# Optimization experiments

Measured on AMD Instinct MI355X. Metric: run time of the kernel, lower is better.

Reference implementation:

```python
import jax, jax.numpy as jnp
import numpy as np

B, T, D = 2, 2048, 1024
N_HEADS, N_KV_HEADS = 16, 4
D_HEAD = D // N_HEADS            # 64
N_GROUPS = N_HEADS // N_KV_HEADS  # 4
ROPE_THETA = 10000.0


def _rope_freqs(t, d_head, theta):
    inv = 1.0 / (theta ** (jnp.arange(0, d_head, 2, dtype=jnp.float32) / d_head))  # (d_head/2,)
    ang = jnp.arange(t, dtype=jnp.float32)[:, None] * inv[None, :]                 # (T, d_head/2)
    return jnp.stack([jnp.cos(ang), jnp.sin(ang)], axis=-1)                        # (T, d_head/2, 2)


def _apply_rope(x, freqs):
    # x: (B, T, H, d_head); freqs: (T, d_head/2, 2) = (cos, sin)
    xr = x.reshape(*x.shape[:-1], -1, 2)          # (B,T,H,d/2,2)
    xre, xim = xr[..., 0], xr[..., 1]
    fre = freqs[None, :, None, :, 0]              # (1,T,1,d/2)
    fim = freqs[None, :, None, :, 1]
    outre = xre * fre - xim * fim
    outim = xre * fim + xim * fre
    return jnp.stack([outre, outim], axis=-1).reshape(x.shape)


def setup_inputs() -> dict:
    key = jax.random.key(0)
    ks = jax.random.split(key, 5)
    x = jax.random.normal(ks[0], (B, T, D), dtype=jnp.float32)
    w_q = jax.random.normal(ks[1], (N_HEADS * D_HEAD, D), dtype=jnp.float32) * 0.02
    w_k = jax.random.normal(ks[2], (N_KV_HEADS * D_HEAD, D), dtype=jnp.float32) * 0.02
    w_v = jax.random.normal(ks[3], (N_KV_HEADS * D_HEAD, D), dtype=jnp.float32) * 0.02
    w_o = jax.random.normal(ks[4], (D, N_HEADS * D_HEAD), dtype=jnp.float32) * 0.02
    rope_freqs = _rope_freqs(T, D_HEAD, ROPE_THETA)
    causal = jnp.tril(jnp.ones((T, T), dtype=bool))
    mask = jnp.where(causal, 0.0, -1e9).astype(jnp.float32)[None, None]  # (1,1,T,T)
    return {"x": x, "rope_freqs": rope_freqs, "mask": mask,
            "w_q": w_q, "w_k": w_k, "w_v": w_v, "w_o": w_o}


def reference(x, rope_freqs, mask, w_q, w_k, w_v, w_o):
    # projections (torch Linear: y = x @ W.T)
    q = jnp.einsum('btd,od->bto', x, w_q).reshape(B, T, N_HEADS, D_HEAD)
    k = jnp.einsum('btd,od->bto', x, w_k).reshape(B, T, N_KV_HEADS, D_HEAD)
    v = jnp.einsum('btd,od->bto', x, w_v).reshape(B, T, N_KV_HEADS, D_HEAD)
    q = _apply_rope(q, rope_freqs)
    k = _apply_rope(k, rope_freqs)
    # GQA: expand KV heads (kv head h -> N_GROUPS contiguous query heads)
    k = jnp.repeat(k, N_GROUPS, axis=2)   # (B,T,H,d)
    v = jnp.repeat(v, N_GROUPS, axis=2)
    q = q.transpose(0, 2, 1, 3)           # (B,H,T,d)
    k = k.transpose(0, 2, 1, 3)
    v = v.transpose(0, 2, 1, 3)
    scale = 1.0 / np.sqrt(D_HEAD).astype(np.float32)
    scores = jnp.einsum('bhqd,bhkd->bhqk', q, k) * scale + mask
    attn = jax.nn.softmax(scores, axis=-1)
    out = jnp.einsum('bhqk,bhkd->bhqd', attn, v)
    out = out.transpose(0, 2, 1, 3).reshape(B, T, N_HEADS * D_HEAD)
    return jnp.einsum('bto,do->btd', out, w_o)
```

## Files before the change

### kernel.cpp

```cpp
#include <hip/hip_runtime.h>
#include <hip/hip_bf16.h>
#include <cstddef>
#include <type_traits>

#define TT   2048
#define NH   16
#define NKV  4
#define DH   64

typedef __bf16 bf16x8 __attribute__((ext_vector_type(8)));
typedef float  f32x4  __attribute__((ext_vector_type(4)));

#if __has_builtin(__builtin_amdgcn_exp2f)
#define EXP2F(x) __builtin_amdgcn_exp2f(x)
#else
#define EXP2F(x) __expf((x) * 0.69314718056f)
#endif

#define QSCALE 0.180336880f

__device__ __forceinline__ void gl_lds16(const __bf16* g, __bf16* l)
{
    __builtin_amdgcn_global_load_lds(
        (const __attribute__((address_space(1))) void*)g,
        (__attribute__((address_space(3))) void*)l,
        16, 0, 0);
}

__global__ __launch_bounds__(256)
void cast_kernel(const float* __restrict__ x,  const float* __restrict__ wq,
                 const float* __restrict__ wk, const float* __restrict__ wv,
                 const float* __restrict__ wo,
                 __bf16* __restrict__ xb, __bf16* __restrict__ wqkv,
                 __bf16* __restrict__ wob)
{
    const int g = blockIdx.x * 256 + threadIdx.x;
    const float* src;
    __bf16* dst;
    int off;
    if (g < 1048576)       { src = x;  dst = xb;   off = g; }
    else if (g < 1310720)  { src = wq; dst = wqkv; off = g - 1048576; }
    else if (g < 1376256)  { src = wk; dst = wqkv + 1048576; off = g - 1310720; }
    else if (g < 1441792)  { src = wv; dst = wqkv + 1310720; off = g - 1376256; }
    else                   { src = wo; dst = wob;  off = g - 1441792; }
    const float4 v = *(const float4*)(src + (size_t)off * 4);
    union { __bf16 h[4]; uint2 u; } o;
    o.h[0] = (__bf16)v.x; o.h[1] = (__bf16)v.y;
    o.h[2] = (__bf16)v.z; o.h[3] = (__bf16)v.w;
    *(uint2*)(dst + (size_t)off * 4) = o.u;
}

template<int MODE>
__global__ __launch_bounds__(256, 3)
void mm_kernel(const __bf16* __restrict__ A,
               const __bf16* __restrict__ W,
               const float* __restrict__ rope,
               void* __restrict__ O0, void* __restrict__ O1,
               void* __restrict__ O2)
{
    constexpr int K  = 1024;
    constexpr int NK = K / 32;
    constexpr int NX = (MODE == 0) ? 12 : 8;
    __shared__ __bf16 As[2][64 * 32];
    __shared__ __bf16 Bs[2][128 * 32];

    const int tid  = threadIdx.x;
    const int lane = tid & 63;
    const int wv   = tid >> 6;
    const int quad = lane >> 4;
    const int lc   = lane & 15;
    const int wbase = tid & 192;

    const int dlin = blockIdx.x + NX * blockIdx.y;
    const int nid  = (dlin & 7) * ((NX * 64) >> 3) + (dlin >> 3);
    const int bx   = nid % NX;
    const int by   = nid / NX;

    const int gm0  = by * 64;
    const int gn0  = bx * 128;
    const int wc0  = wv * 32;

    size_t gaA;
    {
        const int p = tid;
        const int r = p >> 2, q = (p & 3) ^ ((r >> 1) & 3);
        gaA = (size_t)r * K + q * 8;
    }
    size_t gaB[2];
#pragma unroll
    for (int j = 0; j < 2; j++) {
        const int p = tid + j * 256;
        const int r = p >> 2, q = (p & 3) ^ ((r >> 1) & 3);
        gaB[j] = (size_t)r * K + q * 8;
    }
    const __bf16* Ag = A + (size_t)gm0 * K;
    const __bf16* Wg = W + (size_t)gn0 * K;

    auto foff = [&](int row) { return (row * 4 + (quad ^ ((row >> 1) & 3))) * 8; };
    int aoff[4], boff[2];
#pragma unroll
    for (int i = 0; i < 4; i++) aoff[i] = foff(i * 16 + lc);
#pragma unroll
    for (int j = 0; j < 2; j++) boff[j] = foff(wc0 + j * 16 + lc);

    f32x4 acc[4][2];
#pragma unroll
    for (int i = 0; i < 4; i++)
#pragma unroll
        for (int j = 0; j < 2; j++) acc[i][j] = (f32x4){0.f, 0.f, 0.f, 0.f};

    auto stage = [&](int s, int kt) {
        const int kb = kt * 32;
        gl_lds16(Ag + gaA + kb, &As[s][wbase * 8]);
        gl_lds16(Wg + gaB[0] + kb, &Bs[s][wbase * 8]);
        gl_lds16(Wg + gaB[1] + kb, &Bs[s][(wbase + 256) * 8]);
    };

    stage(0, 0);
    __syncthreads();

    for (int kt = 0; kt < NK; kt++) {
        const int P = kt & 1;
        if (kt + 1 < NK) stage(P ^ 1, kt + 1);

        bf16x8 af[4], bfr[2];
#pragma unroll
        for (int i = 0; i < 4; i++) af[i]  = *(const bf16x8*)&As[P][aoff[i]];
#pragma unroll
        for (int j = 0; j < 2; j++) bfr[j] = *(const bf16x8*)&Bs[P][boff[j]];
#pragma unroll
        for (int i = 0; i < 4; i++)
#pragma unroll
            for (int j = 0; j < 2; j++)
                acc[i][j] = __builtin_amdgcn_mfma_f32_16x16x32_bf16(
                    af[i], bfr[j], acc[i][j], 0, 0, 0);

        if (kt + 1 < NK) __syncthreads();
    }

    if (MODE == 0) {
        __bf16* Qo = (__bf16*)O0;
        __bf16* Ko = (__bf16*)O1;
        __bf16* Vo = (__bf16*)O2;
        const int region = (gn0 < 1024) ? 0 : (gn0 < 1280) ? 1 : 2;
#pragma unroll
        for (int i = 0; i < 4; i++) {
#pragma unroll
            for (int r = 0; r < 4; r++) {
                const int grow = gm0 + i * 16 + quad * 4 + r;
                const int b = grow >> 11, t = grow & 2047;
                const float* rrow = rope + t * 64;
#pragma unroll
                for (int j = 0; j < 2; j++) {
                    const float v = acc[i][j][r];
                    const float partner = __shfl_xor(v, 1, 64);
                    const int col = gn0 + wc0 + j * 16 + lc;
                    if (region == 0) {
                        const int h = col >> 6, d = col & 63;
                        const float2 cs = *(const float2*)(rrow + (d >> 1) * 2);
                        const float out = v * cs.x + partner * ((d & 1) ? cs.y : -cs.y);
                        Qo[((size_t)(b * NH + h) * TT + t) * DH + d] = (__bf16)(out * QSCALE);
                    } else if (region == 1) {
                        const int ck = col - 1024;
                        const int kh = ck >> 6, d = ck & 63;
                        const float2 cs = *(const float2*)(rrow + (d >> 1) * 2);
                        const float out = v * cs.x + partner * ((d & 1) ? cs.y : -cs.y);
                        Ko[((size_t)(b * NKV + kh) * TT + t) * DH + d] = (__bf16)out;
                    } else {
                        const int cv = col - 1280;
                        const int kh = cv >> 6, d = cv & 63;
                        Vo[((size_t)(b * NKV + kh) * DH + d) * TT + t] = (__bf16)v;
                    }
                }
            }
        }
    } else {
        float* Of = (float*)O0;
#pragma unroll
        for (int i = 0; i < 4; i++)
#pragma unroll
            for (int r = 0; r < 4; r++) {
                const int grow = gm0 + i * 16 + quad * 4 + r;
#pragma unroll
                for (int j = 0; j < 2; j++)
                    Of[(size_t)grow * 1024 + gn0 + wc0 + j * 16 + lc] = acc[i][j][r];
            }
    }
}

__global__ __launch_bounds__(256, 4)
void attn_kernel(const __bf16* __restrict__ Q,
                 const __bf16* __restrict__ K,
                 const __bf16* __restrict__ Vt,
                 __bf16* __restrict__ O)
{
    __shared__ __bf16 Ks[2][64 * 64];
    __shared__ __bf16 Vs[2][64 * 64];
    __shared__ __bf16 Ps[4][16][64];

    const int tid  = threadIdx.x;
    const int lane = tid & 63;
    const int wv   = tid >> 6;
    const int quad = lane >> 4;
    const int lc   = lane & 15;

    const int a   = blockIdx.x & 31;
    const int rep = blockIdx.x >> 5;
    const int qt  = ((rep >> 3) & 1) ? (31 - a) : a;
    const int b   = rep >> 4;
    const int h   = rep & 15;
    const int kh  = h >> 2;
    const int nk  = qt + 1;

    const __bf16* Kg = K  + (size_t)(b * NKV + kh) * TT * DH;
    const __bf16* Vg = Vt + (size_t)(b * NKV + kh) * DH * TT;

    bf16x8 qb[2];
    {
        const __bf16* qp = Q + ((size_t)(b * NH + h) * TT
                                + qt * 64 + wv * 16 + lc) * DH;
        qb[0] = *(const bf16x8*)(qp + quad * 8);
        qb[1] = *(const bf16x8*)(qp + 32 + quad * 8);
    }

    int koff[2], voff[2], lsl[2];
#pragma unroll
    for (int j = 0; j < 2; j++) {
        const int p  = tid + j * 256;
        const int r  = p >> 3;
        const int qs = (p & 7) ^ (r & 7);
        koff[j] = r * DH + qs * 8;
        voff[j] = r * TT + qs * 8;
        lsl[j]  = p * 8;
    }

    int foff[4][2];
#pragma unroll
    for (int g = 0; g < 4; g++)
#pragma unroll
        for (int c = 0; c < 2; c++)
            foff[g][c] = ((g * 16 + lc) * 8 + ((c * 4 + quad) ^ (lc & 7))) * 8;

    const int psw = 2 * (lc & 7);
    char* prow = (char*)&Ps[wv][lc][0];

    float l_s = 0.f;
    f32x4 oacc[4];
#pragma unroll
    for (int g = 0; g < 4; g++) oacc[g] = (f32x4){0.f, 0.f, 0.f, 0.f};

    bf16x8 kr[2], vr[2];
    auto load_regs = [&](int kt) {
        const __bf16* kp = Kg + (size_t)kt * 64 * DH;
        const __bf16* vp = Vg + (size_t)kt * 64;
#pragma unroll
        for (int j = 0; j < 2; j++) {
            kr[j] = *(const bf16x8*)(kp + koff[j]);
            vr[j] = *(const bf16x8*)(vp + voff[j]);
        }
    };
    auto store_lds = [&](int buf) {
#pragma unroll
        for (int j = 0; j < 2; j++) {
            *(bf16x8*)&Ks[buf][lsl[j]] = kr[j];
            *(bf16x8*)&Vs[buf][lsl[j]] = vr[j];
        }
    };

    load_regs(0);
    store_lds(0);
    if (nk > 1) load_regs(1);
    __syncthreads();

    for (int kt = 0; kt < nk; kt++) {
        const int cur = kt & 1;

        bf16x8 ka[4][2];
#pragma unroll
        for (int g = 0; g < 4; g++) {
            ka[g][0] = *(const bf16x8*)&Ks[cur][foff[g][0]];
            ka[g][1] = *(const bf16x8*)&Ks[cur][foff[g][1]];
        }

        if (kt + 1 < nk) store_lds(cur ^ 1);

        const int D = qt * 64 + wv * 16 - kt * 64;

        f32x4 s[4];
        __builtin_amdgcn_s_setprio(1);
#pragma unroll
        for (int g = 0; g < 4; g++) {
            f32x4 z = (f32x4){0.f, 0.f, 0.f, 0.f};
            z = __builtin_amdgcn_mfma_f32_16x16x32_bf16(ka[g][0], qb[0], z, 0, 0, 0);
            z = __builtin_amdgcn_mfma_f32_16x16x32_bf16(ka[g][1], qb[1], z, 0, 0, 0);
            s[g] = z;
        }
        __builtin_amdgcn_s_setprio(0);

        if (D < 63) {
            const int thr = D + lc;
#pragma unroll
            for (int g = 0; g < 4; g++)
#pragma unroll
                for (int r = 0; r < 4; r++)
                    if (g * 16 + quad * 4 + r > thr) s[g][r] = -1e30f;
        }

        float rs = 0.f;
#pragma unroll
        for (int g = 0; g < 4; g++) {
#pragma unroll
            for (int r = 0; r < 4; r++) {
                s[g][r] = EXP2F(s[g][r]);
                rs += s[g][r];
            }
            union { __bf16 hh[4]; uint2 uu; } pk;
            pk.hh[0] = (__bf16)s[g][0]; pk.hh[1] = (__bf16)s[g][1];
            pk.hh[2] = (__bf16)s[g][2]; pk.hh[3] = (__bf16)s[g][3];
            *(uint2*)(prow + ((4 * g + quad) ^ psw) * 8) = pk.uu;
        }
        l_s += rs;

        bf16x8 va[4][2];
#pragma unroll
        for (int g = 0; g < 4; g++) {
            va[g][0] = *(const bf16x8*)&Vs[cur][foff[g][0]];
            va[g][1] = *(const bf16x8*)&Vs[cur][foff[g][1]];
        }

        const bf16x8 pb0 = *(const bf16x8*)(prow + (( 2 * quad) ^ psw) * 8);
        const bf16x8 pb1 = *(const bf16x8*)(prow + ((8 + 2 * quad) ^ psw) * 8);
        __builtin_amdgcn_s_setprio(1);
#pragma unroll
        for (int g = 0; g < 4; g++) {
            oacc[g] = __builtin_amdgcn_mfma_f32_16x16x32_bf16(va[g][0], pb0, oacc[g], 0, 0, 0);
            oacc[g] = __builtin_amdgcn_mfma_f32_16x16x32_bf16(va[g][1], pb1, oacc[g], 0, 0, 0);
        }
        __builtin_amdgcn_s_setprio(0);

        if (kt + 2 < nk) load_regs(kt + 2);
        if (kt + 1 < nk) __syncthreads();
    }

    {
        float l = l_s;
        l += __shfl_xor(l, 16, 64);
        l += __shfl_xor(l, 32, 64);
        const float inv = 1.f / l;
        const int t = qt * 64 + wv * 16 + lc;
        __bf16* op = O + (size_t)(b * TT + t) * (NH * DH) + h * DH;
#pragma unroll
        for (int g = 0; g < 4; g++) {
            union { __bf16 hh[4]; uint2 uu; } pk;
            pk.hh[0] = (__bf16)(oacc[g][0] * inv);
            pk.hh[1] = (__bf16)(oacc[g][1] * inv);
            pk.hh[2] = (__bf16)(oacc[g][2] * inv);
            pk.hh[3] = (__bf16)(oacc[g][3] * inv);
            *(uint2*)(op + g * 16 + quad * 4) = pk.uu;
        }
    }
}

extern "C" void kernel_launch(void* const* d_in, const int* in_sizes, int n_in,
                              void* d_out, int out_size, void* d_ws, size_t ws_size,
                              hipStream_t stream)
{
    const float* x    = (const float*)d_in[0];
    const float* rope = (const float*)d_in[1];
    const float* w_q  = (const float*)d_in[3];
    const float* w_k  = (const float*)d_in[4];
    const float* w_v  = (const float*)d_in[5];
    const float* w_o  = (const float*)d_in[6];
    float* out = (float*)d_out;

    char* ws = (char*)d_ws;
    __bf16* Qb   = (__bf16*)(ws);
    __bf16* Kb   = (__bf16*)(ws + (8  << 20));
    __bf16* Vtb  = (__bf16*)(ws + (10 << 20));
    __bf16* AOb  = (__bf16*)(ws + (12 << 20));
    __bf16* xb   = (__bf16*)(ws + (20 << 20));
    __bf16* Wqkv = (__bf16*)(ws + (28 << 20));
    __bf16* Wob  = (__bf16*)(ws + (31 << 20));

    cast_kernel<<<6656, dim3(256), 0, stream>>>(x, w_q, w_k, w_v, w_o,
                                                xb, Wqkv, Wob);

    dim3 g1(12, 64);
    mm_kernel<0><<<g1, dim3(256), 0, stream>>>(xb, Wqkv, rope,
                                               (void*)Qb, (void*)Kb, (void*)Vtb);

    attn_kernel<<<1024, dim3(256), 0, stream>>>(Qb, Kb, Vtb, AOb);

    dim3 g3(8, 64);
    mm_kernel<1><<<g3, dim3(256), 0, stream>>>(AOb, Wob, rope,
                                               (void*)out, nullptr, nullptr);
}
```

Baseline: 174.8 us.

## Shrink GEMM tiles to 64x64 and replace LDS-direct loads with register-staged pipeline

The projection GEMMs switch from 64x128 tiles to 64x64 tiles, which doubles the number of workgroups and raises the occupancy hint to 4 per CU. The direct global-to-LDS loads are replaced by global loads into registers, prefetched three k-steps ahead and written to a double-buffered LDS, with the loop unrolled by two. The intent is more parallelism across CUs and better hiding of load latency. In exchange, each tile gets less data reuse (more global traffic per MFMA) and the kernel uses more VGPRs.

```diff
diff --git a/kernel.cpp b/kernel.cpp
--- a/kernel.cpp
+++ b/kernel.cpp
@@ -18,14 +18,6 @@
 #endif
 
 #define QSCALE 0.180336880f
-
-__device__ __forceinline__ void gl_lds16(const __bf16* g, __bf16* l)
-{
-    __builtin_amdgcn_global_load_lds(
-        (const __attribute__((address_space(1))) void*)g,
-        (__attribute__((address_space(3))) void*)l,
-        16, 0, 0);
-}
 
 __global__ __launch_bounds__(256)
 void cast_kernel(const float* __restrict__ x,  const float* __restrict__ wq,
@@ -51,7 +43,7 @@
 }
 
 template<int MODE>
-__global__ __launch_bounds__(256, 3)
+__global__ __launch_bounds__(256, 4)
 void mm_kernel(const __bf16* __restrict__ A,
                const __bf16* __restrict__ W,
                const float* __restrict__ rope,
@@ -60,82 +52,83 @@
 {
     constexpr int K  = 1024;
     constexpr int NK = K / 32;
-    constexpr int NX = (MODE == 0) ? 12 : 8;
+    constexpr int NX = (MODE == 0) ? 24 : 16;
+    constexpr int NWG = NX * 64;
     __shared__ __bf16 As[2][64 * 32];
-    __shared__ __bf16 Bs[2][128 * 32];
+    __shared__ __bf16 Bs[2][64 * 32];
 
     const int tid  = threadIdx.x;
     const int lane = tid & 63;
     const int wv   = tid >> 6;
     const int quad = lane >> 4;
     const int lc   = lane & 15;
-    const int wbase = tid & 192;
 
     const int dlin = blockIdx.x + NX * blockIdx.y;
-    const int nid  = (dlin & 7) * ((NX * 64) >> 3) + (dlin >> 3);
+    const int nid  = (dlin & 7) * (NWG >> 3) + (dlin >> 3);
     const int bx   = nid % NX;
     const int by   = nid / NX;
 
     const int gm0  = by * 64;
-    const int gn0  = bx * 128;
-    const int wc0  = wv * 32;
-
-    size_t gaA;
+    const int gn0  = bx * 64;
+    const int wc0  = wv * 16;
+
+    int gaA, lsA;
     {
         const int p = tid;
         const int r = p >> 2, q = (p & 3) ^ ((r >> 1) & 3);
-        gaA = (size_t)r * K + q * 8;
-    }
-    size_t gaB[2];
-#pragma unroll
-    for (int j = 0; j < 2; j++) {
-        const int p = tid + j * 256;
-        const int r = p >> 2, q = (p & 3) ^ ((r >> 1) & 3);
-        gaB[j] = (size_t)r * K + q * 8;
-    }
+        gaA = r * K + q * 8;
+        lsA = p * 8;
+    }
+    const int gaB = gaA, lsB = lsA;
     const __bf16* Ag = A + (size_t)gm0 * K;
     const __bf16* Wg = W + (size_t)gn0 * K;
 
     auto foff = [&](int row) { return (row * 4 + (quad ^ ((row >> 1) & 3))) * 8; };
-    int aoff[4], boff[2];
+    int aoff[4], boff;
 #pragma unroll
     for (int i = 0; i < 4; i++) aoff[i] = foff(i * 16 + lc);
-#pragma unroll
-    for (int j = 0; j < 2; j++) boff[j] = foff(wc0 + j * 16 + lc);
-
-    f32x4 acc[4][2];
-#pragma unroll
-    for (int i = 0; i < 4; i++)
-#pragma unroll
-        for (int j = 0; j < 2; j++) acc[i][j] = (f32x4){0.f, 0.f, 0.f, 0.f};
-
-    auto stage = [&](int s, int kt) {
+    boff = foff(wc0 + lc);
+
+    f32x4 acc[4];
+#pragma unroll
+    for (int i = 0; i < 4; i++) acc[i] = (f32x4){0.f, 0.f, 0.f, 0.f};
+
+    bf16x8 ar[2], br[2];
+
+    auto load_set = [&](int kt, int s) {
         const int kb = kt * 32;
-        gl_lds16(Ag + gaA + kb, &As[s][wbase * 8]);
-        gl_lds16(Wg + gaB[0] + kb, &Bs[s][wbase * 8]);
-        gl_lds16(Wg + gaB[1] + kb, &Bs[s][(wbase + 256) * 8]);
-    };
-
-    stage(0, 0);
+        ar[s] = *(const bf16x8*)(Ag + gaA + kb);
+        br[s] = *(const bf16x8*)(Wg + gaB + kb);
+    };
+    auto store_set = [&](int s) {
+        *(bf16x8*)&As[s][lsA] = ar[s];
+        *(bf16x8*)&Bs[s][lsB] = br[s];
+    };
+
+    load_set(0, 0);
+    store_set(0);
+    load_set(1, 1);
+    load_set(2, 0);
     __syncthreads();
 
-    for (int kt = 0; kt < NK; kt++) {
-        const int P = kt & 1;
-        if (kt + 1 < NK) stage(P ^ 1, kt + 1);
-
-        bf16x8 af[4], bfr[2];
-#pragma unroll
-        for (int i = 0; i < 4; i++) af[i]  = *(const bf16x8*)&As[P][aoff[i]];
-#pragma unroll
-        for (int j = 0; j < 2; j++) bfr[j] = *(const bf16x8*)&Bs[P][boff[j]];
+    auto step = [&](int kt, auto pc) {
+        constexpr int P = decltype(pc)::value;
+        constexpr int Q = 1 - P;
+        bf16x8 af[4], bfr;
+#pragma unroll
+        for (int i = 0; i < 4; i++) af[i] = *(const bf16x8*)&As[P][aoff[i]];
+        bfr = *(const bf16x8*)&Bs[P][boff];
+        if (kt + 1 < NK) store_set(Q);
 #pragma unroll
         for (int i = 0; i < 4; i++)
-#pragma unroll
-            for (int j = 0; j < 2; j++)
-                acc[i][j] = __builtin_amdgcn_mfma_f32_16x16x32_bf16(
-                    af[i], bfr[j], acc[i][j], 0, 0, 0);
-
+            acc[i] = __builtin_amdgcn_mfma_f32_16x16x32_bf16(
+                af[i], bfr, acc[i], 0, 0, 0);
+        if (kt + 3 < NK) load_set(kt + 3, Q);
         if (kt + 1 < NK) __syncthreads();
+    };
+    for (int kt = 0; kt < NK; kt += 2) {
+        step(kt,     std::integral_constant<int, 0>{});
+        step(kt + 1, std::integral_constant<int, 1>{});
     }
 
     if (MODE == 0) {
@@ -150,27 +143,24 @@
                 const int grow = gm0 + i * 16 + quad * 4 + r;
                 const int b = grow >> 11, t = grow & 2047;
                 const float* rrow = rope + t * 64;
-#pragma unroll
-                for (int j = 0; j < 2; j++) {
-                    const float v = acc[i][j][r];
-                    const float partner = __shfl_xor(v, 1, 64);
-                    const int col = gn0 + wc0 + j * 16 + lc;
-                    if (region == 0) {
-                        const int h = col >> 6, d = col & 63;
-                        const float2 cs = *(const float2*)(rrow + (d >> 1) * 2);
-                        const float out = v * cs.x + partner * ((d & 1) ? cs.y : -cs.y);
-                        Qo[((size_t)(b * NH + h) * TT + t) * DH + d] = (__bf16)(out * QSCALE);
-                    } else if (region == 1) {
-                        const int ck = col - 1024;
-                        const int kh = ck >> 6, d = ck & 63;
-                        const float2 cs = *(const float2*)(rrow + (d >> 1) * 2);
-                        const float out = v * cs.x + partner * ((d & 1) ? cs.y : -cs.y);
-                        Ko[((size_t)(b * NKV + kh) * TT + t) * DH + d] = (__bf16)out;
-                    } else {
-                        const int cv = col - 1280;
-                        const int kh = cv >> 6, d = cv & 63;
-                        Vo[((size_t)(b * NKV + kh) * DH + d) * TT + t] = (__bf16)v;
-                    }
+                const float v = acc[i][r];
+                const float partner = __shfl_xor(v, 1, 64);
+                const int col = gn0 + wc0 + lc;
+                if (region == 0) {
+                    const int h = col >> 6, d = col & 63;
+                    const float2 cs = *(const float2*)(rrow + (d >> 1) * 2);
+                    const float out = v * cs.x + partner * ((d & 1) ? cs.y : -cs.y);
+                    Qo[((size_t)(b * NH + h) * TT + t) * DH + d] = (__bf16)(out * QSCALE);
+                } else if (region == 1) {
+                    const int ck = col - 1024;
+                    const int kh = ck >> 6, d = ck & 63;
+                    const float2 cs = *(const float2*)(rrow + (d >> 1) * 2);
+                    const float out = v * cs.x + partner * ((d & 1) ? cs.y : -cs.y);
+                    Ko[((size_t)(b * NKV + kh) * TT + t) * DH + d] = (__bf16)out;
+                } else {
+                    const int cv = col - 1280;
+                    const int kh = cv >> 6, d = cv & 63;
+                    Vo[((size_t)(b * NKV + kh) * DH + d) * TT + t] = (__bf16)v;
                 }
             }
         }
@@ -181,9 +171,7 @@
 #pragma unroll
             for (int r = 0; r < 4; r++) {
                 const int grow = gm0 + i * 16 + quad * 4 + r;
-#pragma unroll
-                for (int j = 0; j < 2; j++)
-                    Of[(size_t)grow * 1024 + gn0 + wc0 + j * 16 + lc] = acc[i][j][r];
+                Of[(size_t)grow * 1024 + gn0 + wc0 + lc] = acc[i][r];
             }
     }
 }
@@ -385,13 +373,13 @@
     cast_kernel<<<6656, dim3(256), 0, stream>>>(x, w_q, w_k, w_v, w_o,
                                                 xb, Wqkv, Wob);
 
-    dim3 g1(12, 64);
+    dim3 g1(24, 64);
     mm_kernel<0><<<g1, dim3(256), 0, stream>>>(xb, Wqkv, rope,
                                                (void*)Qb, (void*)Kb, (void*)Vtb);
 
     attn_kernel<<<1024, dim3(256), 0, stream>>>(Qb, Kb, Vtb, AOb);
 
-    dim3 g3(8, 64);
+    dim3 g3(16, 64);
     mm_kernel<1><<<g3, dim3(256), 0, stream>>>(AOb, Wob, rope,
                                                (void*)out, nullptr, nullptr);
 }
```

After: 176.2 us. No clear change (+0.8%).
